# Optimization experiments

Measured on AMD Instinct MI355X. Metric: run time of the kernel, lower is better.

## Reference

```python
import jax, jax.numpy as jnp
import numpy as np

EMBED = 768
HEADS = 12
HEAD_DIM = EMBED // HEADS
HIDDEN = 4 * EMBED
EPS = 1e-5


def _layernorm(x, w, b):
    mu = jnp.mean(x, axis=-1, keepdims=True)
    var = jnp.mean(jnp.square(x - mu), axis=-1, keepdims=True)
    return (x - mu) * jax.lax.rsqrt(var + EPS) * w + b


def setup_inputs() -> dict:
    key = jax.random.key(0)
    ks = jax.random.split(key, 12)
    s = 0.02
    return {
        "x": jax.random.normal(ks[0], (2, 2048, EMBED), dtype=jnp.float32),
        "ln1_w": jnp.ones((EMBED,), jnp.float32),
        "ln1_b": jnp.zeros((EMBED,), jnp.float32),
        "qkv_w": jax.random.normal(ks[1], (3 * EMBED, EMBED), jnp.float32) * s,
        "qkv_b": jnp.zeros((3 * EMBED,), jnp.float32),
        "proj_w": jax.random.normal(ks[2], (EMBED, EMBED), jnp.float32) * s,
        "proj_b": jnp.zeros((EMBED,), jnp.float32),
        "ln2_w": jnp.ones((EMBED,), jnp.float32),
        "ln2_b": jnp.zeros((EMBED,), jnp.float32),
        "fc1_w": jax.random.normal(ks[3], (HIDDEN, EMBED), jnp.float32) * s,
        "fc1_b": jnp.zeros((HIDDEN,), jnp.float32),
        "fc2_w": jax.random.normal(ks[4], (EMBED, HIDDEN), jnp.float32) * s,
        "fc2_b": jnp.zeros((EMBED,), jnp.float32),
    }


def reference(x, ln1_w, ln1_b, qkv_w, qkv_b, proj_w, proj_b,
              ln2_w, ln2_b, fc1_w, fc1_b, fc2_w, fc2_b):
    B, N, C = x.shape
    scale = float(HEAD_DIM) ** 0.5  # NOTE: module MULTIPLIES by sqrt(head_dim)

    # --- attention branch ---
    h = _layernorm(x, ln1_w, ln1_b)
    qkv = h @ qkv_w.T + qkv_b                     # [B,N,3C]
    qkv = qkv.reshape(B, N, 3, HEADS, HEAD_DIM)
    q = qkv[:, :, 0].transpose(0, 2, 1, 3)        # [B,H,N,D]
    k = qkv[:, :, 1].transpose(0, 2, 1, 3)
    v = qkv[:, :, 2].transpose(0, 2, 1, 3)
    attn = jnp.einsum('bhnd,bhmd->bhnm', q, k) * scale
    attn = jax.nn.softmax(attn, axis=-1)
    o = jnp.einsum('bhnm,bhmd->bhnd', attn, v)    # [B,H,N,D]
    o = o.transpose(0, 2, 1, 3).reshape(B, N, C)
    x = x + (o @ proj_w.T + proj_b)

    # --- MLP branch ---
    h = _layernorm(x, ln2_w, ln2_b)
    h = jax.nn.gelu(h @ fc1_w.T + fc1_b, approximate=False)
    x = x + (h @ fc2_w.T + fc2_b)
    return x
```

## Files before the change

kernel.cpp:

```cpp
#include <hip/hip_runtime.h>
#include <hip/hip_bf16.h>

typedef __attribute__((ext_vector_type(8))) short short8;
typedef __attribute__((ext_vector_type(4))) float f32x4;
typedef __attribute__((ext_vector_type(4))) int i32x4;

__device__ inline unsigned short f2bs(float f) {
  union { float f; unsigned u; } v; v.f = f;
  unsigned r = v.u + 0x7fff + ((v.u >> 16) & 1);
  return (unsigned short)(r >> 16);
}

__device__ inline unsigned pkbf(float a, float b) {
  __hip_bfloat162 h = __float22bfloat162_rn(float2{a, b});
  union { __hip_bfloat162 h; unsigned u; } c; c.h = h;
  return c.u;
}

__device__ inline float exp2v(float x) {
  float r; asm("v_exp_f32 %0, %1" : "=v"(r) : "v"(x)); return r;
}

__device__ inline float max3f(float a, float b, float c) {
  return fmaxf(fmaxf(a, b), c);
}

__device__ inline void gload16(const void* g, void* l) {
  __builtin_amdgcn_global_load_lds((const __attribute__((address_space(1))) void*)g,
                                   (__attribute__((address_space(3))) void*)l,
                                   16, 0, 0);
}

__global__ __launch_bounds__(256)
void cvt_all(const float* __restrict__ s0, const float* __restrict__ s1,
             const float* __restrict__ s2, const float* __restrict__ s3,
             unsigned short* __restrict__ d0, unsigned short* __restrict__ d1,
             unsigned short* __restrict__ d2, unsigned short* __restrict__ d3)
{
  size_t i = (size_t)blockIdx.x * 256 + threadIdx.x;
  const float* src; unsigned short* dst;
  if (i < 442368) { src = s0; dst = d0; }
  else if (i < 589824) { src = s1; dst = d1; i -= 442368; }
  else if (i < 1179648) { src = s2; dst = d2; i -= 589824; }
  else { src = s3; dst = d3; i -= 1179648; }
  float4 v = ((const float4*)src)[i];
  ushort4 o;
  o.x = f2bs(v.x); o.y = f2bs(v.y); o.z = f2bs(v.z); o.w = f2bs(v.w);
  ((ushort4*)dst)[i] = o;
}

__global__ __launch_bounds__(256)
void ln_kernel(const float* __restrict__ x, const float* __restrict__ w,
               const float* __restrict__ bsh, unsigned short* __restrict__ out)
{
  const int row = blockIdx.x;
  const float* xr = x + (size_t)row * 768;
  float v[3];
  float s = 0.f, sq = 0.f;
#pragma unroll
  for (int i = 0; i < 3; ++i) {
    v[i] = xr[threadIdx.x + i * 256];
    s += v[i]; sq += v[i] * v[i];
  }
#pragma unroll
  for (int d = 1; d < 64; d <<= 1) {
    s  += __shfl_xor(s, d, 64);
    sq += __shfl_xor(sq, d, 64);
  }
  __shared__ float ss[4], ssq[4];
  const int wv = threadIdx.x >> 6;
  if ((threadIdx.x & 63) == 0) { ss[wv] = s; ssq[wv] = sq; }
  __syncthreads();
  s  = ss[0] + ss[1] + ss[2] + ss[3];
  sq = ssq[0] + ssq[1] + ssq[2] + ssq[3];
  const float mu = s * (1.0f / 768.0f);
  const float var = sq * (1.0f / 768.0f) - mu * mu;
  const float rstd = rsqrtf(var + 1e-5f);
#pragma unroll
  for (int i = 0; i < 3; ++i) {
    const int c = threadIdx.x + i * 256;
    out[(size_t)row * 768 + c] = f2bs((v[i] - mu) * rstd * w[c] + bsh[c]);
  }
}

__global__ __launch_bounds__(256)
void reduce_ln2(const float* __restrict__ p, const float* __restrict__ bias,
                const float* __restrict__ resid, const float* __restrict__ lw,
                const float* __restrict__ lb, float* __restrict__ x2,
                unsigned short* __restrict__ h)
{
  const size_t MN = 4096ull * 768;
  const int row = blockIdx.x;
  const size_t r0 = (size_t)row * 768;
  float v[3];
  float s = 0.f, sq = 0.f;
#pragma unroll
  for (int i = 0; i < 3; ++i) {
    const int c = threadIdx.x + i * 256;
    const float a = p[r0 + c] + p[MN + r0 + c] + bias[c] + resid[r0 + c];
    x2[r0 + c] = a;
    v[i] = a; s += a; sq += a * a;
  }
#pragma unroll
  for (int d = 1; d < 64; d <<= 1) {
    s  += __shfl_xor(s, d, 64);
    sq += __shfl_xor(sq, d, 64);
  }
  __shared__ float ss[4], ssq[4];
  const int wv = threadIdx.x >> 6;
  if ((threadIdx.x & 63) == 0) { ss[wv] = s; ssq[wv] = sq; }
  __syncthreads();
  s  = ss[0] + ss[1] + ss[2] + ss[3];
  sq = ssq[0] + ssq[1] + ssq[2] + ssq[3];
  const float mu = s * (1.0f / 768.0f);
  const float var = sq * (1.0f / 768.0f) - mu * mu;
  const float rstd = rsqrtf(var + 1e-5f);
#pragma unroll
  for (int i = 0; i < 3; ++i) {
    const int c = threadIdx.x + i * 256;
    h[r0 + c] = f2bs((v[i] - mu) * rstd * lw[c] + lb[c]);
  }
}

template<int S>
__global__ __launch_bounds__(256)
void reduce_k(const float* __restrict__ p, const float* __restrict__ bias,
              const float* __restrict__ resid, float* __restrict__ out)
{
  const size_t MN = 4096ull * 768;
  const size_t i = ((size_t)blockIdx.x * 256 + threadIdx.x) * 4;
  float4 a = *(const float4*)(p + i);
#pragma unroll
  for (int s = 1; s < S; ++s) {
    float4 b = *(const float4*)(p + s * MN + i);
    a.x += b.x; a.y += b.y; a.z += b.z; a.w += b.w;
  }
  const int col = (int)(i % 768);
  float4 bb = *(const float4*)(bias + col);
  float4 rr = *(const float4*)(resid + i);
  a.x += bb.x + rr.x; a.y += bb.y + rr.y; a.z += bb.z + rr.z; a.w += bb.w + rr.w;
  *(float4*)(out + i) = a;
}

template<int EPI>
__global__ __launch_bounds__(256, 3)
void gemm_nt(const unsigned short* __restrict__ A,
             const unsigned short* __restrict__ Bw,
             const float* __restrict__ bias,
             const float* __restrict__ resid,
             void* __restrict__ out0, void* __restrict__ out1, void* __restrict__ out2,
             int M, int N, int Kslice, int Kstride)
{
  __shared__ __align__(16) unsigned short As[3][128 * 32];
  __shared__ __align__(16) unsigned short Bs[3][128 * 32];
  const int tid = threadIdx.x;
  const int lane = tid & 63;
  const int w = tid >> 6;
  const int wr = w >> 1, wc = w & 1;
  const int l15 = lane & 15, g = lane >> 4;

  const int nwg = gridDim.x * gridDim.y;
  const int hw = blockIdx.y * gridDim.x + blockIdx.x;
  const int virt = (hw & 7) * (nwg >> 3) + (hw >> 3);
  const int m0 = (virt / gridDim.x) * 128;
  const int n0 = (virt % gridDim.x) * 128;
  const int kbase = blockIdx.z * Kslice;

  f32x4 acc[4][4];
#pragma unroll
  for (int m = 0; m < 4; ++m)
#pragma unroll
    for (int n = 0; n < 4; ++n)
      acc[m][n] = (f32x4){0.f, 0.f, 0.f, 0.f};

  auto stage = [&](int buf, int k0) {
#pragma unroll
    for (int i = 0; i < 2; ++i) {
      const int f = tid + i * 256;
      const int row = f >> 2, c8 = f & 3;
      const int sc = c8 ^ (row & 3);
      gload16(A  + (size_t)(m0 + row) * Kstride + kbase + k0 + sc * 8, (char*)&As[buf][0] + f * 16);
      gload16(Bw + (size_t)(n0 + row) * Kstride + kbase + k0 + sc * 8, (char*)&Bs[buf][0] + f * 16);
    }
  };

  const int NT = Kslice >> 5;
  stage(0, 0);
  stage(1, 32);

  for (int t = 0; t < NT; ++t) {
    const int buf = t % 3;
    if (t + 1 < NT) {
      asm volatile("s_waitcnt vmcnt(4)" ::: "memory");
    } else {
      asm volatile("s_waitcnt vmcnt(0)" ::: "memory");
    }
    __builtin_amdgcn_s_barrier();
    asm volatile("" ::: "memory");
    if (t + 2 < NT) stage((t + 2) % 3, (t + 2) * 32);

    short8 af[4], bfr[4];
#pragma unroll
    for (int m = 0; m < 4; ++m) {
      const int r = wr * 64 + m * 16 + l15;
      af[m] = *(const short8*)((const char*)&As[buf][0] + ((size_t)r * 32 + (g ^ (r & 3)) * 8) * 2);
    }
#pragma unroll
    for (int n = 0; n < 4; ++n) {
      const int r = wc * 64 + n * 16 + l15;
      bfr[n] = *(const short8*)((const char*)&Bs[buf][0] + ((size_t)r * 32 + (g ^ (r & 3)) * 8) * 2);
    }
#pragma unroll
    for (int m = 0; m < 4; ++m)
#pragma unroll
      for (int n = 0; n < 4; ++n)
        acc[m][n] = __builtin_amdgcn_mfma_f32_16x16x32_bf16(af[m], bfr[n], acc[m][n], 0, 0, 0);
    asm volatile("" ::: "memory");
  }

#pragma unroll
  for (int m = 0; m < 4; ++m) {
    const int gmBase = m0 + wr * 64 + m * 16 + g * 4;
#pragma unroll
    for (int n = 0; n < 4; ++n) {
      const int gn = n0 + wc * 64 + n * 16 + l15;
      const float bval = (EPI == 4) ? 0.0f : bias[gn];
      float vj[4];
#pragma unroll
      for (int j = 0; j < 4; ++j) vj[j] = acc[m][n][j] + bval;
      if (EPI == 0) {
        const int three = gn / 768;
        const int hh = (gn % 768) >> 6;
        const int d = gn & 63;
        const int bb = gmBase >> 11, t = gmBase & 2047;
        if (three == 2) {
          ushort4 pk;
          pk.x = f2bs(vj[0]); pk.y = f2bs(vj[1]); pk.z = f2bs(vj[2]); pk.w = f2bs(vj[3]);
          const int kt = t & 63;
          const size_t pos = ((((size_t)(bb * 12 + hh) * 32 + (t >> 6)) * 8 + (d >> 4) * 2 + (kt >> 5)) * 64
                              + ((kt >> 2) & 3) * 16 + (d & 15)) * 8 + ((kt >> 4) & 1) * 4;
          *(ushort4*)((unsigned short*)out2 + pos) = pk;
        } else {
          unsigned short* dst = (three == 0) ? (unsigned short*)out0 : (unsigned short*)out1;
#pragma unroll
          for (int j = 0; j < 4; ++j) {
            float v = vj[j];
            if (three == 0) v *= 11.5415603f;
            dst[(((size_t)bb * 12 + hh) * 2048 + (t + j)) * 64 + d] = f2bs(v);
          }
        }
      } else if (EPI == 1 || EPI == 3) {
#pragma unroll
        for (int j = 0; j < 4; ++j) {
          const int gm = gmBase + j;
          ((float*)out0)[(size_t)gm * N + gn] = vj[j] + resid[(size_t)gm * N + gn];
        }
      } else if (EPI == 2) {
#pragma unroll
        for (int j = 0; j < 4; ++j) {
          const int gm = gmBase + j;
          const float vv = vj[j];
          const float u = vv * (1.0f + 0.044715f * vv * vv);
          const float E = exp2v(2.0f * 0.7978845608f * 1.4426950409f * u);
          const float ge = vv - vv / (1.0f + E);
          ((unsigned short*)out0)[(size_t)gm * N + gn] = f2bs(ge);
        }
      } else {
        float* po = (float*)out0 + (size_t)blockIdx.z * M * N;
#pragma unroll
        for (int j = 0; j < 4; ++j) {
          const int gm = gmBase + j;
          po[(size_t)gm * N + gn] = vj[j];
        }
      }
    }
  }
}

__global__ __launch_bounds__(256, 3)
void attn_fwd(const unsigned short* __restrict__ Q,
              const unsigned short* __restrict__ K,
              const unsigned short* __restrict__ Vf,
              unsigned short* __restrict__ O)
{
  __shared__ __align__(1024) unsigned short Ks[3][4096];
  __shared__ __align__(1024) unsigned short Vs[3][4096];
  const int tid = threadIdx.x, lane = tid & 63, w = tid >> 6;
  const int l15 = lane & 15, g = lane >> 4;

  const int hw = blockIdx.y * gridDim.x + blockIdx.x;
  const int virt = (hw & 7) * 96 + (hw >> 3);
  const int qblk = virt & 31;
  const int bh = virt >> 5;
  const int b = bh / 12, h = bh % 12;
  const int q0 = qblk * 64;
  const unsigned short* Qb = Q  + (size_t)bh * 2048 * 64;
  const unsigned short* Kb = K  + (size_t)bh * 2048 * 64;
  const unsigned short* Vb = Vf + (size_t)bh * 2048 * 64;

  const int qr = q0 + w * 16 + l15;
  short8 qf[2];
  qf[0] = *(const short8*)(Qb + (size_t)qr * 64 + g * 8);
  qf[1] = *(const short8*)(Qb + (size_t)qr * 64 + 32 + g * 8);

  float m_run = -1e30f, l_part = 0.f;
  f32x4 o_acc[4];
#pragma unroll
  for (int dc = 0; dc < 4; ++dc) o_acc[dc] = (f32x4){0.f, 0.f, 0.f, 0.f};

  auto stage = [&](int buf, int tIdx) {
    const int kb = tIdx * 64;
#pragma unroll
    for (int i = 0; i < 2; ++i) {
      const int f = w * 2 + i;
      const int n = f >> 1, kc = f & 1;
      gload16(Kb + (size_t)(kb + n * 16 + l15) * 64 + kc * 32 + g * 8,
              (char*)&Ks[buf][0] + f * 1024);
    }
#pragma unroll
    for (int i = 0; i < 2; ++i) {
      const int chunk = tid + i * 256;
      gload16(Vb + (size_t)tIdx * 4096 + chunk * 8,
              (char*)&Vs[buf][0] + chunk * 16);
    }
  };

  stage(0, 0);
  stage(1, 1);

  for (int t = 0; t < 32; ++t) {
    const int buf = t % 3;
    if (t < 31) {
      asm volatile("s_waitcnt vmcnt(4)" ::: "memory");
    } else {
      asm volatile("s_waitcnt vmcnt(0)" ::: "memory");
    }
    __builtin_amdgcn_s_barrier();
    asm volatile("" ::: "memory");
    if (t < 30) stage((t + 2) % 3, t + 2);

    f32x4 s2[4];
#pragma unroll
    for (int n = 0; n < 4; ++n) s2[n] = (f32x4){0.f, 0.f, 0.f, 0.f};
    __builtin_amdgcn_s_setprio(1);
#pragma unroll
    for (int n = 0; n < 4; ++n) {
      short8 kf0 = *(const short8*)(&Ks[buf][(n * 2 + 0) * 512 + lane * 8]);
      short8 kf1 = *(const short8*)(&Ks[buf][(n * 2 + 1) * 512 + lane * 8]);
      s2[n] = __builtin_amdgcn_mfma_f32_16x16x32_bf16(kf0, qf[0], s2[n], 0, 0, 0);
      s2[n] = __builtin_amdgcn_mfma_f32_16x16x32_bf16(kf1, qf[1], s2[n], 0, 0, 0);
    }
    __builtin_amdgcn_s_setprio(0);

    float mx = max3f(max3f(s2[0][0], s2[0][1], s2[0][2]),
                     max3f(s2[0][3], s2[1][0], s2[1][1]),
                     max3f(s2[1][2], s2[1][3], s2[2][0]));
    mx = max3f(mx, max3f(s2[2][1], s2[2][2], s2[2][3]),
                   max3f(s2[3][0], s2[3][1], fmaxf(s2[3][2], s2[3][3])));
    mx = fmaxf(mx, __shfl_xor(mx, 16, 64));
    mx = fmaxf(mx, __shfl_xor(mx, 32, 64));
    if (__any(mx > m_run + 8.0f)) {
      const float mn = fmaxf(m_run, mx);
      const float alpha = exp2v(m_run - mn);
      m_run = mn;
      l_part *= alpha;
#pragma unroll
      for (int j = 0; j < 4; ++j) {
        const float aB = __shfl(alpha, (lane & 48) | (g * 4 + j), 64);
#pragma unroll
        for (int dc = 0; dc < 4; ++dc) o_acc[dc][j] *= aB;
      }
    }
    float e[4][4];
    float rs = 0.f;
#pragma unroll
    for (int n = 0; n < 4; ++n)
#pragma unroll
      for (int j = 0; j < 4; ++j) {
        e[n][j] = exp2v(s2[n][j] - m_run);
        rs += e[n][j];
      }
    l_part += rs;

    unsigned pw[2][4];
#pragma unroll
    for (int kc = 0; kc < 2; ++kc) {
      pw[kc][0] = pkbf(e[2 * kc][0],     e[2 * kc][1]);
      pw[kc][1] = pkbf(e[2 * kc][2],     e[2 * kc][3]);
      pw[kc][2] = pkbf(e[2 * kc + 1][0], e[2 * kc + 1][1]);
      pw[kc][3] = pkbf(e[2 * kc + 1][2], e[2 * kc + 1][3]);
    }

    const char* vsb = (const char*)&Vs[buf][0];
    __builtin_amdgcn_s_setprio(1);
#pragma unroll
    for (int kc = 0; kc < 2; ++kc) {
      i32x4 pt; pt.x = (int)pw[kc][0]; pt.y = (int)pw[kc][1]; pt.z = (int)pw[kc][2]; pt.w = (int)pw[kc][3];
      short8 pf = *(short8*)&pt;
#pragma unroll
      for (int dc = 0; dc < 4; ++dc) {
        short8 vfr = *(const short8*)(vsb + (((dc * 2 + kc) * 64 + lane) * 16));
        o_acc[dc] = __builtin_amdgcn_mfma_f32_16x16x32_bf16(pf, vfr, o_acc[dc], 0, 0, 0);
      }
    }
    __builtin_amdgcn_s_setprio(0);
    asm volatile("" ::: "memory");
  }

  l_part += __shfl_xor(l_part, 16, 64);
  l_part += __shfl_xor(l_part, 32, 64);
#pragma unroll
  for (int j = 0; j < 4; ++j) {
    const float lB = __shfl(l_part, (lane & 48) | (g * 4 + j), 64);
    const float inv = 1.0f / lB;
    const int qrow = q0 + w * 16 + g * 4 + j;
#pragma unroll
    for (int dc = 0; dc < 4; ++dc) {
      O[((size_t)b * 2048 + qrow) * 768 + h * 64 + dc * 16 + l15] = f2bs(o_acc[dc][j] * inv);
    }
  }
}

extern "C" void kernel_launch(void* const* d_in, const int* in_sizes, int n_in,
                              void* d_out, int out_size, void* d_ws, size_t ws_size,
                              hipStream_t stream)
{
  const float* x      = (const float*)d_in[0];
  const float* ln1_w  = (const float*)d_in[1];
  const float* ln1_b  = (const float*)d_in[2];
  const float* qkv_w  = (const float*)d_in[3];
  const float* qkv_b  = (const float*)d_in[4];
  const float* proj_w = (const float*)d_in[5];
  const float* proj_b = (const float*)d_in[6];
  const float* ln2_w  = (const float*)d_in[7];
  const float* ln2_b  = (const float*)d_in[8];
  const float* fc1_w  = (const float*)d_in[9];
  const float* fc1_b  = (const float*)d_in[10];
  const float* fc2_w  = (const float*)d_in[11];
  const float* fc2_b  = (const float*)d_in[12];

  char* base = (char*)d_ws;
  size_t off = 0;
  auto take = [&](size_t bytes) {
    void* r = base + off;
    off = (off + bytes + 255) & ~(size_t)255;
    return r;
  };
  unsigned short* wq = (unsigned short*)take(2304ull * 768 * 2);
  unsigned short* wp = (unsigned short*)take(768ull * 768 * 2);
  unsigned short* w1 = (unsigned short*)take(3072ull * 768 * 2);
  unsigned short* w2 = (unsigned short*)take(768ull * 3072 * 2);
  unsigned short* h  = (unsigned short*)take(4096ull * 768 * 2);
  float* x2          = (float*)take(4096ull * 768 * 4);
  char* big          = (char*)take(4096ull * 3072 * 2);
  unsigned short* Qb = (unsigned short*)big;
  unsigned short* Kb = (unsigned short*)(big + 4096ull * 768 * 2);
  unsigned short* Vb = (unsigned short*)(big + 2ull * 4096 * 768 * 2);
  unsigned short* a2 = (unsigned short*)big;
  float* part        = (float*)take(4ull * 4096 * 768 * 4);
  const bool can_split = off <= ws_size;

  cvt_all<<<6912, 256, 0, stream>>>(qkv_w, proj_w, fc1_w, fc2_w, wq, wp, w1, w2);

  ln_kernel<<<4096, 256, 0, stream>>>(x, ln1_w, ln1_b, h);
  gemm_nt<0><<<dim3(18, 32), 256, 0, stream>>>(h, wq, qkv_b, nullptr, Qb, Kb, Vb, 4096, 2304, 768, 768);
  attn_fwd<<<dim3(32, 24), 256, 0, stream>>>(Qb, Kb, Vb, h);

  if (can_split) {
    gemm_nt<4><<<dim3(6, 32, 2), 256, 0, stream>>>(h, wp, nullptr, nullptr, part, nullptr, nullptr, 4096, 768, 384, 768);
    reduce_ln2<<<4096, 256, 0, stream>>>(part, proj_b, x, ln2_w, ln2_b, x2, h);
  } else {
    gemm_nt<1><<<dim3(6, 32), 256, 0, stream>>>(h, wp, proj_b, x, x2, nullptr, nullptr, 4096, 768, 768, 768);
    ln_kernel<<<4096, 256, 0, stream>>>(x2, ln2_w, ln2_b, h);
  }

  gemm_nt<2><<<dim3(24, 32), 256, 0, stream>>>(h, w1, fc1_b, nullptr, a2, nullptr, nullptr, 4096, 3072, 768, 768);

  if (can_split) {
    gemm_nt<4><<<dim3(6, 32, 4), 256, 0, stream>>>(a2, w2, nullptr, nullptr, part, nullptr, nullptr, 4096, 768, 768, 3072);
    reduce_k<4><<<3072, 256, 0, stream>>>(part, fc2_b, x2, (float*)d_out);
  } else {
    gemm_nt<3><<<dim3(6, 32), 256, 0, stream>>>(a2, w2, fc2_b, x2, d_out, nullptr, nullptr, 4096, 768, 3072, 3072);
  }
}
```

Baseline: 194.7 us.

## Process two query tiles per wave in attention with 128-thread blocks

The attention kernel now uses 2 waves per block instead of 4, with each wave handling two 16-row query tiles that share the same K and V fragments read from LDS. This halves LDS reads of K/V per query row and doubles the MFMA work per LDS load. Each wave now issues twice as many global-to-LDS loads per stage, and the vmcnt threshold is adjusted to match. The cost is higher register pressure, two independent softmax states per wave, and fewer waves per block to hide latency.

```diff
diff --git a/kernel.cpp b/kernel.cpp
--- a/kernel.cpp
+++ b/kernel.cpp
@@ -277,7 +277,7 @@
   }
 }
 
-__global__ __launch_bounds__(256, 3)
+__global__ __launch_bounds__(128, 2)
 void attn_fwd(const unsigned short* __restrict__ Q,
               const unsigned short* __restrict__ K,
               const unsigned short* __restrict__ Vf,
@@ -298,30 +298,33 @@
   const unsigned short* Kb = K  + (size_t)bh * 2048 * 64;
   const unsigned short* Vb = Vf + (size_t)bh * 2048 * 64;
 
-  const int qr = q0 + w * 16 + l15;
-  short8 qf[2];
-  qf[0] = *(const short8*)(Qb + (size_t)qr * 64 + g * 8);
-  qf[1] = *(const short8*)(Qb + (size_t)qr * 64 + 32 + g * 8);
-
-  float m_run = -1e30f, l_part = 0.f;
-  f32x4 o_acc[4];
-#pragma unroll
-  for (int dc = 0; dc < 4; ++dc) o_acc[dc] = (f32x4){0.f, 0.f, 0.f, 0.f};
+  const int qra = q0 + w * 32 + l15;
+  const int qrb = qra + 16;
+  short8 qfa[2], qfb[2];
+  qfa[0] = *(const short8*)(Qb + (size_t)qra * 64 + g * 8);
+  qfa[1] = *(const short8*)(Qb + (size_t)qra * 64 + 32 + g * 8);
+  qfb[0] = *(const short8*)(Qb + (size_t)qrb * 64 + g * 8);
+  qfb[1] = *(const short8*)(Qb + (size_t)qrb * 64 + 32 + g * 8);
+
+  float m_a = -1e30f, m_b = -1e30f, l_a = 0.f, l_b = 0.f;
+  f32x4 oa[4], ob[4];
+#pragma unroll
+  for (int dc = 0; dc < 4; ++dc) { oa[dc] = (f32x4){0.f,0.f,0.f,0.f}; ob[dc] = (f32x4){0.f,0.f,0.f,0.f}; }
 
   auto stage = [&](int buf, int tIdx) {
     const int kb = tIdx * 64;
 #pragma unroll
-    for (int i = 0; i < 2; ++i) {
-      const int f = w * 2 + i;
+    for (int i = 0; i < 4; ++i) {
+      const int f = w * 4 + i;
       const int n = f >> 1, kc = f & 1;
       gload16(Kb + (size_t)(kb + n * 16 + l15) * 64 + kc * 32 + g * 8,
               (char*)&Ks[buf][0] + f * 1024);
     }
 #pragma unroll
-    for (int i = 0; i < 2; ++i) {
-      const int chunk = tid + i * 256;
-      gload16(Vb + (size_t)tIdx * 4096 + chunk * 8,
-              (char*)&Vs[buf][0] + chunk * 16);
+    for (int i = 0; i < 4; ++i) {
+      const int c = w * 4 + i;
+      gload16(Vb + (size_t)tIdx * 4096 + c * 512 + lane * 8,
+              (char*)&Vs[buf][0] + c * 1024);
     }
   };
 
@@ -331,7 +334,7 @@
   for (int t = 0; t < 32; ++t) {
     const int buf = t % 3;
     if (t < 31) {
-      asm volatile("s_waitcnt vmcnt(4)" ::: "memory");
+      asm volatile("s_waitcnt vmcnt(8)" ::: "memory");
     } else {
       asm volatile("s_waitcnt vmcnt(0)" ::: "memory");
     }
@@ -339,84 +342,127 @@
     asm volatile("" ::: "memory");
     if (t < 30) stage((t + 2) % 3, t + 2);
 
-    f32x4 s2[4];
-#pragma unroll
-    for (int n = 0; n < 4; ++n) s2[n] = (f32x4){0.f, 0.f, 0.f, 0.f};
+    f32x4 sa[4], sb[4];
+#pragma unroll
+    for (int n = 0; n < 4; ++n) { sa[n] = (f32x4){0.f,0.f,0.f,0.f}; sb[n] = (f32x4){0.f,0.f,0.f,0.f}; }
     __builtin_amdgcn_s_setprio(1);
 #pragma unroll
     for (int n = 0; n < 4; ++n) {
       short8 kf0 = *(const short8*)(&Ks[buf][(n * 2 + 0) * 512 + lane * 8]);
       short8 kf1 = *(const short8*)(&Ks[buf][(n * 2 + 1) * 512 + lane * 8]);
-      s2[n] = __builtin_amdgcn_mfma_f32_16x16x32_bf16(kf0, qf[0], s2[n], 0, 0, 0);
-      s2[n] = __builtin_amdgcn_mfma_f32_16x16x32_bf16(kf1, qf[1], s2[n], 0, 0, 0);
+      sa[n] = __builtin_amdgcn_mfma_f32_16x16x32_bf16(kf0, qfa[0], sa[n], 0, 0, 0);
+      sa[n] = __builtin_amdgcn_mfma_f32_16x16x32_bf16(kf1, qfa[1], sa[n], 0, 0, 0);
+      sb[n] = __builtin_amdgcn_mfma_f32_16x16x32_bf16(kf0, qfb[0], sb[n], 0, 0, 0);
+      sb[n] = __builtin_amdgcn_mfma_f32_16x16x32_bf16(kf1, qfb[1], sb[n], 0, 0, 0);
     }
     __builtin_amdgcn_s_setprio(0);
 
-    float mx = max3f(max3f(s2[0][0], s2[0][1], s2[0][2]),
-                     max3f(s2[0][3], s2[1][0], s2[1][1]),
-                     max3f(s2[1][2], s2[1][3], s2[2][0]));
-    mx = max3f(mx, max3f(s2[2][1], s2[2][2], s2[2][3]),
-                   max3f(s2[3][0], s2[3][1], fmaxf(s2[3][2], s2[3][3])));
-    mx = fmaxf(mx, __shfl_xor(mx, 16, 64));
-    mx = fmaxf(mx, __shfl_xor(mx, 32, 64));
-    if (__any(mx > m_run + 8.0f)) {
-      const float mn = fmaxf(m_run, mx);
-      const float alpha = exp2v(m_run - mn);
-      m_run = mn;
-      l_part *= alpha;
-#pragma unroll
-      for (int j = 0; j < 4; ++j) {
-        const float aB = __shfl(alpha, (lane & 48) | (g * 4 + j), 64);
-#pragma unroll
-        for (int dc = 0; dc < 4; ++dc) o_acc[dc][j] *= aB;
+    unsigned pwa[2][4], pwb[2][4];
+    {
+      float mx = max3f(max3f(sa[0][0], sa[0][1], sa[0][2]),
+                       max3f(sa[0][3], sa[1][0], sa[1][1]),
+                       max3f(sa[1][2], sa[1][3], sa[2][0]));
+      mx = max3f(mx, max3f(sa[2][1], sa[2][2], sa[2][3]),
+                     max3f(sa[3][0], sa[3][1], fmaxf(sa[3][2], sa[3][3])));
+      mx = fmaxf(mx, __shfl_xor(mx, 16, 64));
+      mx = fmaxf(mx, __shfl_xor(mx, 32, 64));
+      if (__any(mx > m_a + 8.0f)) {
+        const float mn = fmaxf(m_a, mx);
+        const float alpha = exp2v(m_a - mn);
+        m_a = mn;
+        l_a *= alpha;
+#pragma unroll
+        for (int j = 0; j < 4; ++j) {
+          const float aB = __shfl(alpha, (lane & 48) | (g * 4 + j), 64);
+#pragma unroll
+          for (int dc = 0; dc < 4; ++dc) oa[dc][j] *= aB;
+        }
       }
-    }
-    float e[4][4];
-    float rs = 0.f;
-#pragma unroll
-    for (int n = 0; n < 4; ++n)
-#pragma unroll
-      for (int j = 0; j < 4; ++j) {
-        e[n][j] = exp2v(s2[n][j] - m_run);
-        rs += e[n][j];
+      float e[4][4];
+      float rs = 0.f;
+#pragma unroll
+      for (int n = 0; n < 4; ++n)
+#pragma unroll
+        for (int j = 0; j < 4; ++j) { e[n][j] = exp2v(sa[n][j] - m_a); rs += e[n][j]; }
+      l_a += rs;
+#pragma unroll
+      for (int kc = 0; kc < 2; ++kc) {
+        pwa[kc][0] = pkbf(e[2*kc][0],   e[2*kc][1]);
+        pwa[kc][1] = pkbf(e[2*kc][2],   e[2*kc][3]);
+        pwa[kc][2] = pkbf(e[2*kc+1][0], e[2*kc+1][1]);
+        pwa[kc][3] = pkbf(e[2*kc+1][2], e[2*kc+1][3]);
       }
-    l_part += rs;
-
-    unsigned pw[2][4];
-#pragma unroll
-    for (int kc = 0; kc < 2; ++kc) {
-      pw[kc][0] = pkbf(e[2 * kc][0],     e[2 * kc][1]);
-      pw[kc][1] = pkbf(e[2 * kc][2],     e[2 * kc][3]);
-      pw[kc][2] = pkbf(e[2 * kc + 1][0], e[2 * kc + 1][1]);
-      pw[kc][3] = pkbf(e[2 * kc + 1][2], e[2 * kc + 1][3]);
+    }
+    {
+      float mx = max3f(max3f(sb[0][0], sb[0][1], sb[0][2]),
+                       max3f(sb[0][3], sb[1][0], sb[1][1]),
+                       max3f(sb[1][2], sb[1][3], sb[2][0]));
+      mx = max3f(mx, max3f(sb[2][1], sb[2][2], sb[2][3]),
+                     max3f(sb[3][0], sb[3][1], fmaxf(sb[3][2], sb[3][3])));
+      mx = fmaxf(mx, __shfl_xor(mx, 16, 64));
+      mx = fmaxf(mx, __shfl_xor(mx, 32, 64));
+      if (__any(mx > m_b + 8.0f)) {
+        const float mn = fmaxf(m_b, mx);
+        const float alpha = exp2v(m_b - mn);
+        m_b = mn;
+        l_b *= alpha;
+#pragma unroll
+        for (int j = 0; j < 4; ++j) {
+          const float aB = __shfl(alpha, (lane & 48) | (g * 4 + j), 64);
+#pragma unroll
+          for (int dc = 0; dc < 4; ++dc) ob[dc][j] *= aB;
+        }
+      }
+      float e[4][4];
+      float rs = 0.f;
+#pragma unroll
+      for (int n = 0; n < 4; ++n)
+#pragma unroll
+        for (int j = 0; j < 4; ++j) { e[n][j] = exp2v(sb[n][j] - m_b); rs += e[n][j]; }
+      l_b += rs;
+#pragma unroll
+      for (int kc = 0; kc < 2; ++kc) {
+        pwb[kc][0] = pkbf(e[2*kc][0],   e[2*kc][1]);
+        pwb[kc][1] = pkbf(e[2*kc][2],   e[2*kc][3]);
+        pwb[kc][2] = pkbf(e[2*kc+1][0], e[2*kc+1][1]);
+        pwb[kc][3] = pkbf(e[2*kc+1][2], e[2*kc+1][3]);
+      }
     }
 
     const char* vsb = (const char*)&Vs[buf][0];
     __builtin_amdgcn_s_setprio(1);
 #pragma unroll
     for (int kc = 0; kc < 2; ++kc) {
-      i32x4 pt; pt.x = (int)pw[kc][0]; pt.y = (int)pw[kc][1]; pt.z = (int)pw[kc][2]; pt.w = (int)pw[kc][3];
-      short8 pf = *(short8*)&pt;
+      i32x4 pta; pta.x = (int)pwa[kc][0]; pta.y = (int)pwa[kc][1]; pta.z = (int)pwa[kc][2]; pta.w = (int)pwa[kc][3];
+      i32x4 ptb; ptb.x = (int)pwb[kc][0]; ptb.y = (int)pwb[kc][1]; ptb.z = (int)pwb[kc][2]; ptb.w = (int)pwb[kc][3];
+      short8 pfa = *(short8*)&pta;
+      short8 pfb = *(short8*)&ptb;
 #pragma unroll
       for (int dc = 0; dc < 4; ++dc) {
         short8 vfr = *(const short8*)(vsb + (((dc * 2 + kc) * 64 + lane) * 16));
-        o_acc[dc] = __builtin_amdgcn_mfma_f32_16x16x32_bf16(pf, vfr, o_acc[dc], 0, 0, 0);
+        oa[dc] = __builtin_amdgcn_mfma_f32_16x16x32_bf16(pfa, vfr, oa[dc], 0, 0, 0);
+        ob[dc] = __builtin_amdgcn_mfma_f32_16x16x32_bf16(pfb, vfr, ob[dc], 0, 0, 0);
       }
     }
     __builtin_amdgcn_s_setprio(0);
     asm volatile("" ::: "memory");
   }
 
-  l_part += __shfl_xor(l_part, 16, 64);
-  l_part += __shfl_xor(l_part, 32, 64);
+  l_a += __shfl_xor(l_a, 16, 64);
+  l_a += __shfl_xor(l_a, 32, 64);
+  l_b += __shfl_xor(l_b, 16, 64);
+  l_b += __shfl_xor(l_b, 32, 64);
 #pragma unroll
   for (int j = 0; j < 4; ++j) {
-    const float lB = __shfl(l_part, (lane & 48) | (g * 4 + j), 64);
-    const float inv = 1.0f / lB;
-    const int qrow = q0 + w * 16 + g * 4 + j;
+    const int src = (lane & 48) | (g * 4 + j);
+    const float invA = 1.0f / __shfl(l_a, src, 64);
+    const float invB = 1.0f / __shfl(l_b, src, 64);
+    const int rowA = q0 + w * 32 + g * 4 + j;
+    const int rowB = rowA + 16;
 #pragma unroll
     for (int dc = 0; dc < 4; ++dc) {
-      O[((size_t)b * 2048 + qrow) * 768 + h * 64 + dc * 16 + l15] = f2bs(o_acc[dc][j] * inv);
+      O[((size_t)b * 2048 + rowA) * 768 + h * 64 + dc * 16 + l15] = f2bs(oa[dc][j] * invA);
+      O[((size_t)b * 2048 + rowB) * 768 + h * 64 + dc * 16 + l15] = f2bs(ob[dc][j] * invB);
     }
   }
 }
@@ -464,7 +510,7 @@
 
   ln_kernel<<<4096, 256, 0, stream>>>(x, ln1_w, ln1_b, h);
   gemm_nt<0><<<dim3(18, 32), 256, 0, stream>>>(h, wq, qkv_b, nullptr, Qb, Kb, Vb, 4096, 2304, 768, 768);
-  attn_fwd<<<dim3(32, 24), 256, 0, stream>>>(Qb, Kb, Vb, h);
+  attn_fwd<<<dim3(32, 24), 128, 0, stream>>>(Qb, Kb, Vb, h);
 
   if (can_split) {
     gemm_nt<4><<<dim3(6, 32, 2), 256, 0, stream>>>(h, wp, nullptr, nullptr, part, nullptr, nullptr, 4096, 768, 384, 768);
```

Result: slower. 207.8 us (+6.7%).

## Split attention along KV into two halves and merge with a combine kernel

Applied to the files above, without the earlier changes.

Attention now runs as a split-KV (flash-decoding style) pass: each block handles half of the key/value tiles, writes unnormalized fp32 partial outputs plus running max and sum to workspace, and a new combine kernel rescales and merges the two halves into bf16. LDS staging drops from triple to double buffering, and launch bounds rise to 5 blocks per CU. The goal is to double the number of attention blocks for better CU fill and occupancy. The cost is an extra kernel launch, extra fp32 partial traffic, and a shallower prefetch pipeline that now waits for all loads each iteration.

```diff
diff --git a/kernel.cpp b/kernel.cpp
--- a/kernel.cpp
+++ b/kernel.cpp
@@ -277,14 +277,16 @@
   }
 }
 
-__global__ __launch_bounds__(256, 3)
+template<int SPLIT>
+__global__ __launch_bounds__(256, 5)
 void attn_fwd(const unsigned short* __restrict__ Q,
               const unsigned short* __restrict__ K,
               const unsigned short* __restrict__ Vf,
-              unsigned short* __restrict__ O)
-{
-  __shared__ __align__(1024) unsigned short Ks[3][4096];
-  __shared__ __align__(1024) unsigned short Vs[3][4096];
+              unsigned short* __restrict__ O,
+              float* __restrict__ Op, float* __restrict__ Mb, float* __restrict__ Lb)
+{
+  __shared__ __align__(1024) unsigned short Ks[2][4096];
+  __shared__ __align__(1024) unsigned short Vs[2][4096];
   const int tid = threadIdx.x, lane = tid & 63, w = tid >> 6;
   const int l15 = lane & 15, g = lane >> 4;
 
@@ -294,6 +296,9 @@
   const int bh = virt >> 5;
   const int b = bh / 12, h = bh % 12;
   const int q0 = qblk * 64;
+  const int half = SPLIT ? blockIdx.z : 0;
+  const int NT = SPLIT ? 16 : 32;
+  const int T0 = half * 16;
   const unsigned short* Qb = Q  + (size_t)bh * 2048 * 64;
   const unsigned short* Kb = K  + (size_t)bh * 2048 * 64;
   const unsigned short* Vb = Vf + (size_t)bh * 2048 * 64;
@@ -308,8 +313,8 @@
 #pragma unroll
   for (int dc = 0; dc < 4; ++dc) o_acc[dc] = (f32x4){0.f, 0.f, 0.f, 0.f};
 
-  auto stage = [&](int buf, int tIdx) {
-    const int kb = tIdx * 64;
+  auto stage = [&](int buf, int gt) {
+    const int kb = gt * 64;
 #pragma unroll
     for (int i = 0; i < 2; ++i) {
       const int f = w * 2 + i;
@@ -320,24 +325,19 @@
 #pragma unroll
     for (int i = 0; i < 2; ++i) {
       const int chunk = tid + i * 256;
-      gload16(Vb + (size_t)tIdx * 4096 + chunk * 8,
+      gload16(Vb + (size_t)gt * 4096 + chunk * 8,
               (char*)&Vs[buf][0] + chunk * 16);
     }
   };
 
-  stage(0, 0);
-  stage(1, 1);
-
-  for (int t = 0; t < 32; ++t) {
-    const int buf = t % 3;
-    if (t < 31) {
-      asm volatile("s_waitcnt vmcnt(4)" ::: "memory");
-    } else {
-      asm volatile("s_waitcnt vmcnt(0)" ::: "memory");
-    }
+  stage(0, T0);
+
+  for (int t = 0; t < NT; ++t) {
+    const int buf = t & 1;
+    asm volatile("s_waitcnt vmcnt(0)" ::: "memory");
     __builtin_amdgcn_s_barrier();
     asm volatile("" ::: "memory");
-    if (t < 30) stage((t + 2) % 3, t + 2);
+    if (t + 1 < NT) stage(buf ^ 1, T0 + t + 1);
 
     f32x4 s2[4];
 #pragma unroll
@@ -409,16 +409,56 @@
 
   l_part += __shfl_xor(l_part, 16, 64);
   l_part += __shfl_xor(l_part, 32, 64);
-#pragma unroll
-  for (int j = 0; j < 4; ++j) {
-    const float lB = __shfl(l_part, (lane & 48) | (g * 4 + j), 64);
-    const float inv = 1.0f / lB;
-    const int qrow = q0 + w * 16 + g * 4 + j;
-#pragma unroll
-    for (int dc = 0; dc < 4; ++dc) {
-      O[((size_t)b * 2048 + qrow) * 768 + h * 64 + dc * 16 + l15] = f2bs(o_acc[dc][j] * inv);
-    }
-  }
+  if (SPLIT) {
+    const int rowBase = (half * 24 + bh) * 2048;
+    if (g == 0) {
+      const int qm = q0 + w * 16 + l15;
+      Mb[rowBase + qm] = m_run;
+      Lb[rowBase + qm] = l_part;
+    }
+#pragma unroll
+    for (int j = 0; j < 4; ++j) {
+      const int row = q0 + w * 16 + g * 4 + j;
+#pragma unroll
+      for (int dc = 0; dc < 4; ++dc)
+        Op[(size_t)(rowBase + row) * 64 + dc * 16 + l15] = o_acc[dc][j];
+    }
+  } else {
+#pragma unroll
+    for (int j = 0; j < 4; ++j) {
+      const float lB = __shfl(l_part, (lane & 48) | (g * 4 + j), 64);
+      const float inv = 1.0f / lB;
+      const int qrow = q0 + w * 16 + g * 4 + j;
+#pragma unroll
+      for (int dc = 0; dc < 4; ++dc)
+        O[((size_t)b * 2048 + qrow) * 768 + h * 64 + dc * 16 + l15] = f2bs(o_acc[dc][j] * inv);
+    }
+  }
+}
+
+__global__ __launch_bounds__(256)
+void attn_combine(const float* __restrict__ Op, const float* __restrict__ Mb,
+                  const float* __restrict__ Lb, unsigned short* __restrict__ O)
+{
+  const int idx = blockIdx.x * 256 + threadIdx.x;
+  const int e4 = idx * 4;
+  const int row = e4 >> 6;
+  const int d0 = e4 & 63;
+  const float m1 = Mb[row], m2 = Mb[49152 + row];
+  const float l1 = Lb[row], l2 = Lb[49152 + row];
+  const float mm = fmaxf(m1, m2);
+  const float w1 = exp2v(m1 - mm), w2 = exp2v(m2 - mm);
+  const float inv = 1.0f / (l1 * w1 + l2 * w2);
+  const float4 o1 = *(const float4*)(Op + (size_t)row * 64 + d0);
+  const float4 o2 = *(const float4*)(Op + 49152ull * 64 + (size_t)row * 64 + d0);
+  ushort4 r;
+  r.x = f2bs((o1.x * w1 + o2.x * w2) * inv);
+  r.y = f2bs((o1.y * w1 + o2.y * w2) * inv);
+  r.z = f2bs((o1.z * w1 + o2.z * w2) * inv);
+  r.w = f2bs((o1.w * w1 + o2.w * w2) * inv);
+  const int bh = row >> 11, q = row & 2047;
+  const int b = bh / 12, hh = bh % 12;
+  *(ushort4*)(O + ((size_t)(b * 2048 + q)) * 768 + hh * 64 + d0) = r;
 }
 
 extern "C" void kernel_launch(void* const* d_in, const int* in_sizes, int n_in,
@@ -458,13 +498,21 @@
   unsigned short* Vb = (unsigned short*)(big + 2ull * 4096 * 768 * 2);
   unsigned short* a2 = (unsigned short*)big;
   float* part        = (float*)take(4ull * 4096 * 768 * 4);
+  float* Mb_         = (float*)take(2ull * 49152 * 4);
+  float* Lb_         = (float*)take(2ull * 49152 * 4);
   const bool can_split = off <= ws_size;
 
   cvt_all<<<6912, 256, 0, stream>>>(qkv_w, proj_w, fc1_w, fc2_w, wq, wp, w1, w2);
 
   ln_kernel<<<4096, 256, 0, stream>>>(x, ln1_w, ln1_b, h);
   gemm_nt<0><<<dim3(18, 32), 256, 0, stream>>>(h, wq, qkv_b, nullptr, Qb, Kb, Vb, 4096, 2304, 768, 768);
-  attn_fwd<<<dim3(32, 24), 256, 0, stream>>>(Qb, Kb, Vb, h);
+
+  if (can_split) {
+    attn_fwd<1><<<dim3(32, 24, 2), 256, 0, stream>>>(Qb, Kb, Vb, nullptr, part, Mb_, Lb_);
+    attn_combine<<<3072, 256, 0, stream>>>(part, Mb_, Lb_, h);
+  } else {
+    attn_fwd<0><<<dim3(32, 24), 256, 0, stream>>>(Qb, Kb, Vb, h, nullptr, nullptr, nullptr);
+  }
 
   if (can_split) {
     gemm_nt<4><<<dim3(6, 32, 2), 256, 0, stream>>>(h, wp, nullptr, nullptr, part, nullptr, nullptr, 4096, 768, 384, 768);
```

New measurement: 202.2 us. 1.04x slower.
